# Optimization experiments

Hardware: AMD Instinct MI355X
Metric: run time of the kernel (lower is better)

Reference implementation:

```python
import jax, jax.numpy as jnp
import numpy as np

N = 4096        # batch_size per view
D = 256         # embed_dim
TEMPERATURE = 0.1


def setup_inputs() -> dict:
    key = jax.random.key(0)
    k1, k2 = jax.random.split(key)
    return {
        "z_i": jax.random.normal(k1, (N, D), dtype=jnp.float32),
        "z_j": jax.random.normal(k2, (N, D), dtype=jnp.float32),
    }


def reference(z_i, z_j):
    n = z_i.shape[0]
    # L2-normalize each row (CosineSimilarity == dot of normalized vectors)
    zi = z_i * jax.lax.rsqrt(jnp.sum(z_i * z_i, axis=1, keepdims=True))
    zj = z_j * jax.lax.rsqrt(jnp.sum(z_j * z_j, axis=1, keepdims=True))
    r = jnp.concatenate([zj, zi], axis=0)               # [2n, d], order matches torch cat([z_j, z_i])
    S = (r @ r.T) / TEMPERATURE                          # [2n, 2n] normalized GEMM, no O(n^2 d) broadcast

    idx = jnp.arange(2 * n)
    pos_col = (idx + n) % (2 * n)                        # positive partner: diag(+n) / diag(-n)
    pos = S[idx, pos_col]                                # [2n]

    # Faithful mask: the original masks the diagonal AND both full cross blocks,
    # so negatives are same-view off-diagonal entries only. Keep = negatives + positive.
    same_block = (idx[:, None] // n) == (idx[None, :] // n)
    keep = (same_block & (idx[:, None] != idx[None, :])) | (idx[None, :] == pos_col[:, None])

    # CrossEntropy with label 0 and reduction='sum', then / (2n)  ==  mean(logsumexp - pos)
    lse = jax.nn.logsumexp(jnp.where(keep, S, -jnp.inf), axis=1)  # [2n]
    return jnp.mean(lse - pos)
```

## Files before the change

kernel.cpp:

```cpp
#include <hip/hip_runtime.h>
#include <math.h>

#define N_ROWS 4096
#define DIM 256
constexpr float INV_T = 10.0f;

#define NT 32
#define NTILES 528
#define TOTAL_BLOCKS (2 * NTILES)
#define BM 128
#define BK 64

typedef __attribute__((ext_vector_type(8))) short short8;
typedef __attribute__((ext_vector_type(4))) float floatx4;

__device__ __forceinline__ unsigned short f2bf(float f) {
    unsigned int u = __float_as_uint(f);
    return (unsigned short)((u + 0x7FFFu + ((u >> 16) & 1u)) >> 16);
}

__global__ __launch_bounds__(256) void normalize_kernel(
    const float* __restrict__ z_i, const float* __restrict__ z_j,
    unsigned short* __restrict__ R0, unsigned short* __restrict__ R1,
    float* __restrict__ pos, unsigned int* __restrict__ zero_region)
{
    int gid = blockIdx.x * 256 + threadIdx.x;
    if (gid < 2 * N_ROWS + 1) zero_region[gid] = 0u;

    int wave = threadIdx.x >> 6;
    int lane = threadIdx.x & 63;
    int row = blockIdx.x * 4 + wave;

    float4 a = ((const float4*)(z_i + (size_t)row * DIM))[lane];
    float4 b = ((const float4*)(z_j + (size_t)row * DIM))[lane];

    float ssa = a.x*a.x + a.y*a.y + a.z*a.z + a.w*a.w;
    float ssb = b.x*b.x + b.y*b.y + b.z*b.z + b.w*b.w;
    float dab = a.x*b.x + a.y*b.y + a.z*b.z + a.w*b.w;
    #pragma unroll
    for (int off = 1; off < 64; off <<= 1) {
        ssa += __shfl_xor(ssa, off);
        ssb += __shfl_xor(ssb, off);
        dab += __shfl_xor(dab, off);
    }
    float ra = rsqrtf(ssa);
    float rb = rsqrtf(ssb);

    ushort4 ua, ub;
    ua.x = f2bf(a.x * ra); ua.y = f2bf(a.y * ra); ua.z = f2bf(a.z * ra); ua.w = f2bf(a.w * ra);
    ub.x = f2bf(b.x * rb); ub.y = f2bf(b.y * rb); ub.z = f2bf(b.z * rb); ub.w = f2bf(b.w * rb);
    ((ushort4*)(R1 + (size_t)row * DIM))[lane] = ua;
    ((ushort4*)(R0 + (size_t)row * DIM))[lane] = ub;

    if (lane == 0) pos[row] = dab * ra * rb * INV_T;
}

__global__ __launch_bounds__(256) void gemm_sym(
    const unsigned short* __restrict__ R0,
    const unsigned short* __restrict__ R1,
    float* __restrict__ denom,
    const float* __restrict__ pos,
    float* __restrict__ out)
{
    __shared__ unsigned short As[BM * BK];
    __shared__ unsigned short Bs[BM * BK];
    __shared__ int lastFlag;
    __shared__ float red[4];

    int view = blockIdx.y;
    const unsigned short* R = view ? R1 : R0;
    float* den = denom + view * N_ROWS;

    int t = blockIdx.x;
    int by = 0;
    while (t >= NT - by) { t -= NT - by; ++by; }
    int bx = by + t;
    int rT = by * BM, cT = bx * BM;

    int tid = threadIdx.x;
    int lane = tid & 63;
    int wave = tid >> 6;
    int wy = wave >> 1, wx = wave & 1;
    int m = lane & 15, q = lane >> 4;

    floatx4 acc[4][4] = {};

    for (int kidx = 0; kidx < 4; ++kidx) {
        int k0 = kidx * BK;
        __syncthreads();
        #pragma unroll
        for (int it = 0; it < 4; ++it) {
            int s = it * 256 + tid;
            int row = s >> 3, c = s & 7;
            uint4 va = *(const uint4*)(R + (size_t)(rT + row) * DIM + k0 + c * 8);
            uint4 vb = *(const uint4*)(R + (size_t)(cT + row) * DIM + k0 + c * 8);
            int slot = row * 8 + (c ^ (row & 7));
            *(uint4*)&As[slot * 8] = va;
            *(uint4*)&Bs[slot * 8] = vb;
        }
        __syncthreads();

        #pragma unroll
        for (int kk = 0; kk < 2; ++kk) {
            short8 af[4], bfr[4];
            #pragma unroll
            for (int tt = 0; tt < 4; ++tt) {
                int ra = wy * 64 + tt * 16 + m;
                af[tt] = *(const short8*)&As[(ra * 8 + ((kk * 4 + q) ^ (ra & 7))) * 8];
                int rb = wx * 64 + tt * 16 + m;
                bfr[tt] = *(const short8*)&Bs[(rb * 8 + ((kk * 4 + q) ^ (rb & 7))) * 8];
            }
            #pragma unroll
            for (int i = 0; i < 4; ++i)
                #pragma unroll
                for (int j = 0; j < 4; ++j)
                    acc[i][j] = __builtin_amdgcn_mfma_f32_16x16x32_bf16(af[i], bfr[j], acc[i][j], 0, 0, 0);
        }
    }

    float rs[4][4] = {};
    float cs[4] = {0.f, 0.f, 0.f, 0.f};
    #pragma unroll
    for (int i = 0; i < 4; ++i) {
        #pragma unroll
        for (int j = 0; j < 4; ++j) {
            int gcol = cT + wx * 64 + j * 16 + m;
            #pragma unroll
            for (int r = 0; r < 4; ++r) {
                int grow = rT + wy * 64 + i * 16 + q * 4 + r;
                float e = (grow == gcol) ? 0.0f : __expf(acc[i][j][r] * INV_T);
                rs[i][r] += e;
                cs[j] += e;
            }
        }
    }
    #pragma unroll
    for (int off = 1; off < 16; off <<= 1)
        #pragma unroll
        for (int i = 0; i < 4; ++i)
            #pragma unroll
            for (int r = 0; r < 4; ++r)
                rs[i][r] += __shfl_xor(rs[i][r], off);
    if (m == 0) {
        #pragma unroll
        for (int i = 0; i < 4; ++i)
            #pragma unroll
            for (int r = 0; r < 4; ++r)
                atomicAdd(&den[rT + wy * 64 + i * 16 + q * 4 + r], rs[i][r]);
    }
    if (bx != by) {
        #pragma unroll
        for (int off = 16; off < 64; off <<= 1)
            #pragma unroll
            for (int j = 0; j < 4; ++j)
                cs[j] += __shfl_xor(cs[j], off);
        if (q == 0) {
            #pragma unroll
            for (int j = 0; j < 4; ++j)
                atomicAdd(&den[cT + wx * 64 + j * 16 + m], cs[j]);
        }
    }

    asm volatile("s_waitcnt vmcnt(0)" ::: "memory");
    __syncthreads();
    int* counter = (int*)(denom + 2 * N_ROWS);
    if (tid == 0) lastFlag = (atomicAdd(counter, 1) == TOTAL_BLOCKS - 1);
    __syncthreads();
    if (lastFlag) {
        float s = 0.f;
        for (int r = tid; r < 2 * N_ROWS; r += 256) {
            float p = pos[r & (N_ROWS - 1)];
            float d = __hip_atomic_load(&denom[r], __ATOMIC_RELAXED, __HIP_MEMORY_SCOPE_AGENT);
            s += __logf(d + __expf(p)) - p;
        }
        #pragma unroll
        for (int off = 1; off < 64; off <<= 1) s += __shfl_xor(s, off);
        if (lane == 0) red[wave] = s;
        __syncthreads();
        if (tid == 0) out[0] = (red[0] + red[1] + red[2] + red[3]) * (1.0f / (2 * N_ROWS));
    }
}

extern "C" void kernel_launch(void* const* d_in, const int* in_sizes, int n_in,
                              void* d_out, int out_size, void* d_ws, size_t ws_size,
                              hipStream_t stream) {
    const float* z_i = (const float*)d_in[0];
    const float* z_j = (const float*)d_in[1];
    char* ws = (char*)d_ws;
    unsigned short* R0 = (unsigned short*)ws;
    unsigned short* R1 = (unsigned short*)(ws + (2u << 20));
    float* pos   = (float*)(ws + (4u << 20));
    float* denom = (float*)(ws + (4u << 20) + (64u << 10));

    normalize_kernel<<<N_ROWS / 4, 256, 0, stream>>>(z_i, z_j, R0, R1, pos,
                                                     (unsigned int*)denom);
    dim3 grid(NTILES, 2);
    gemm_sym<<<grid, 256, 0, stream>>>(R0, R1, denom, pos, (float*)d_out);
}
```

Baseline: 101.9 us.

## Replace global atomics and last-block reduction with per-tile partials and finalize kernel

Each GEMM tile block now writes its row and column exp-sums into its own partial buffer slot instead of atomically adding into a shared denominator array. The last-block detection counter is gone. A separate finalize kernel gathers each row's partials across tiles, computes the log-sum-exp minus the positive, and atomically accumulates the mean. This removes atomic contention and the serial tail done by one block, at the cost of an extra kernel launch and some partial-buffer traffic.

```diff
diff --git a/kernel.cpp b/kernel.cpp
--- a/kernel.cpp
+++ b/kernel.cpp
@@ -7,9 +7,9 @@
 
 #define NT 32
 #define NTILES 528
-#define TOTAL_BLOCKS (2 * NTILES)
 #define BM 128
 #define BK 64
+#define PSTRIDE 512
 
 typedef __attribute__((ext_vector_type(8))) short short8;
 typedef __attribute__((ext_vector_type(4))) float floatx4;
@@ -22,10 +22,9 @@
 __global__ __launch_bounds__(256) void normalize_kernel(
     const float* __restrict__ z_i, const float* __restrict__ z_j,
     unsigned short* __restrict__ R0, unsigned short* __restrict__ R1,
-    float* __restrict__ pos, unsigned int* __restrict__ zero_region)
+    float* __restrict__ pos, float* __restrict__ out)
 {
-    int gid = blockIdx.x * 256 + threadIdx.x;
-    if (gid < 2 * N_ROWS + 1) zero_region[gid] = 0u;
+    if (blockIdx.x == 0 && threadIdx.x == 0) out[0] = 0.0f;
 
     int wave = threadIdx.x >> 6;
     int lane = threadIdx.x & 63;
@@ -58,18 +57,14 @@
 __global__ __launch_bounds__(256) void gemm_sym(
     const unsigned short* __restrict__ R0,
     const unsigned short* __restrict__ R1,
-    float* __restrict__ denom,
-    const float* __restrict__ pos,
-    float* __restrict__ out)
+    float* __restrict__ part)
 {
     __shared__ unsigned short As[BM * BK];
     __shared__ unsigned short Bs[BM * BK];
-    __shared__ int lastFlag;
-    __shared__ float red[4];
 
     int view = blockIdx.y;
     const unsigned short* R = view ? R1 : R0;
-    float* den = denom + view * N_ROWS;
+    float* P = part + (size_t)(view * NTILES + blockIdx.x) * PSTRIDE;
 
     int t = blockIdx.x;
     int by = 0;
@@ -143,42 +138,49 @@
                 rs[i][r] += __shfl_xor(rs[i][r], off);
     if (m == 0) {
         #pragma unroll
-        for (int i = 0; i < 4; ++i)
-            #pragma unroll
-            for (int r = 0; r < 4; ++r)
-                atomicAdd(&den[rT + wy * 64 + i * 16 + q * 4 + r], rs[i][r]);
-    }
-    if (bx != by) {
-        #pragma unroll
-        for (int off = 16; off < 64; off <<= 1)
-            #pragma unroll
-            for (int j = 0; j < 4; ++j)
-                cs[j] += __shfl_xor(cs[j], off);
-        if (q == 0) {
-            #pragma unroll
-            for (int j = 0; j < 4; ++j)
-                atomicAdd(&den[cT + wx * 64 + j * 16 + m], cs[j]);
-        }
-    }
-
-    asm volatile("s_waitcnt vmcnt(0)" ::: "memory");
-    __syncthreads();
-    int* counter = (int*)(denom + 2 * N_ROWS);
-    if (tid == 0) lastFlag = (atomicAdd(counter, 1) == TOTAL_BLOCKS - 1);
-    __syncthreads();
-    if (lastFlag) {
-        float s = 0.f;
-        for (int r = tid; r < 2 * N_ROWS; r += 256) {
-            float p = pos[r & (N_ROWS - 1)];
-            float d = __hip_atomic_load(&denom[r], __ATOMIC_RELAXED, __HIP_MEMORY_SCOPE_AGENT);
-            s += __logf(d + __expf(p)) - p;
-        }
-        #pragma unroll
-        for (int off = 1; off < 64; off <<= 1) s += __shfl_xor(s, off);
-        if (lane == 0) red[wave] = s;
-        __syncthreads();
-        if (tid == 0) out[0] = (red[0] + red[1] + red[2] + red[3]) * (1.0f / (2 * N_ROWS));
-    }
+        for (int i = 0; i < 4; ++i) {
+            float4 v = make_float4(rs[i][0], rs[i][1], rs[i][2], rs[i][3]);
+            *(float4*)&P[wx * 128 + wy * 64 + i * 16 + q * 4] = v;
+        }
+    }
+    #pragma unroll
+    for (int off = 16; off < 64; off <<= 1)
+        #pragma unroll
+        for (int j = 0; j < 4; ++j)
+            cs[j] += __shfl_xor(cs[j], off);
+    if (q == 0) {
+        #pragma unroll
+        for (int j = 0; j < 4; ++j)
+            P[256 + wy * 128 + wx * 64 + j * 16 + m] = (bx == by) ? 0.0f : cs[j];
+    }
+}
+
+__global__ __launch_bounds__(256) void finalize_kernel(
+    const float* __restrict__ part, const float* __restrict__ pos,
+    float* __restrict__ out)
+{
+    int g = blockIdx.x * 256 + threadIdx.x;
+    int v = g >> 12, r = g & (N_ROWS - 1);
+    int b = r >> 7, l = r & 127;
+    const float* P = part + (size_t)v * NTILES * PSTRIDE;
+
+    float d = 0.f;
+    int t0 = b * NT - (b * (b - 1)) / 2;
+    for (int k = 0; k < NT - b; ++k) {
+        const float* T = P + (size_t)(t0 + k) * PSTRIDE;
+        d += T[l] + T[128 + l];
+    }
+    for (int by = 0; by <= b; ++by) {
+        int tb = by * NT - (by * (by - 1)) / 2 + (b - by);
+        const float* T = P + (size_t)tb * PSTRIDE;
+        d += T[256 + l] + T[384 + l];
+    }
+    float p = pos[r];
+    float s = __logf(d + __expf(p)) - p;
+    #pragma unroll
+    for (int off = 1; off < 64; off <<= 1) s += __shfl_xor(s, off);
+    if ((threadIdx.x & 63) == 0)
+        atomicAdd(out, s * (1.0f / (2 * N_ROWS)));
 }
 
 extern "C" void kernel_launch(void* const* d_in, const int* in_sizes, int n_in,
@@ -189,11 +191,12 @@
     char* ws = (char*)d_ws;
     unsigned short* R0 = (unsigned short*)ws;
     unsigned short* R1 = (unsigned short*)(ws + (2u << 20));
-    float* pos   = (float*)(ws + (4u << 20));
-    float* denom = (float*)(ws + (4u << 20) + (64u << 10));
+    float* pos  = (float*)(ws + (4u << 20));
+    float* part = (float*)(ws + (4u << 20) + (64u << 10));
 
     normalize_kernel<<<N_ROWS / 4, 256, 0, stream>>>(z_i, z_j, R0, R1, pos,
-                                                     (unsigned int*)denom);
+                                                     (float*)d_out);
     dim3 grid(NTILES, 2);
-    gemm_sym<<<grid, 256, 0, stream>>>(R0, R1, denom, pos, (float*)d_out);
-}
+    gemm_sym<<<grid, 256, 0, stream>>>(R0, R1, part);
+    finalize_kernel<<<2 * N_ROWS / 256, 256, 0, stream>>>(part, pos, (float*)d_out);
+}
```

Measured after the change: 91.36 us. 1.12x faster.
